# Kernel tuning notes

Measured on AMD Instinct MI355X. Metric: run time of the kernel, lower is better.

Reference implementation:

```python
import jax, jax.numpy as jnp
import numpy as np

N_CLUSTER = 1
SIZE, RATIO = 32, 0.1


def _lin_mat(n_in, n_out):
    # bilinear, align_corners=True interpolation matrix [n_out, n_in]
    src = np.arange(n_out) * (n_in - 1) / (n_out - 1)
    lo = np.floor(src).astype(np.int64)
    hi = np.minimum(lo + 1, n_in - 1)
    w = (src - lo).astype(np.float32)
    M = np.zeros((n_out, n_in), np.float32)
    M[np.arange(n_out), lo] += 1.0 - w
    M[np.arange(n_out), hi] += w
    return jnp.asarray(M)


def setup_inputs() -> dict:
    key = jax.random.key(0)
    ks = jax.random.split(key, 5)
    B, D, H, W, C = 16, 128, 128, 128, 6
    inp = {
        "assp": jax.random.normal(ks[0], (B, D, H, W), jnp.float32),
        "cls_w": jax.random.normal(ks[1], (C, D), jnp.float32) * 0.05,
        "cls_b": jnp.zeros((C,), jnp.float32),
        "key_w": jax.random.normal(ks[2], (128, D), jnp.float32) * 0.05,
        "key_b": jnp.zeros((128,), jnp.float32),
        "query_w": jax.random.normal(ks[3], (C, 128, D), jnp.float32) * 0.05,
        "query_b": jnp.zeros((C, 128), jnp.float32),
    }
    rng = np.random.default_rng(0)
    idx = rng.permutation(SIZE * SIZE)[: int(SIZE * SIZE * RATIO)]  # 102 unique pixels
    inp["px"] = jnp.asarray(idx // SIZE, jnp.int32)
    inp["py"] = jnp.asarray(idx % SIZE, jnp.int32)
    return inp


def reference(assp, cls_w, cls_b, key_w, key_b, query_w, query_b, px, py):
    B, D, H, W = assp.shape
    C = cls_w.shape[0]
    # pseudo labels (torch.no_grad)
    feats = jax.lax.stop_gradient(assp)
    pseudo = jnp.einsum('bdhw,cd->bchw', feats, cls_w) + cls_b[None, :, None, None]
    mask = jnp.argmax(pseudo, axis=1)                      # [B,H,W]
    onehot = jax.nn.one_hot(mask, C, dtype=assp.dtype)      # [B,H,W,C]
    counts = onehot.sum((1, 2))                             # [B,C]
    sums = jnp.einsum('bdhw,bhwc->bcd', assp, onehot)       # masked class sums
    protoC = sums / (counts[..., None] + 1e-5)              # [B,C,D]
    protoC = jnp.where(counts[..., None] > 0, protoC, 0.0)  # zero_prototype fallback
    protos12 = jnp.broadcast_to(protoC[:, :, None, :], (B, C, 2, D)).reshape(B, 2 * C, D)

    # DomainTrain: gather sampled pixels, L2 dist to 12 prototypes, argmin, scatter replace
    feat_px = assp[:, :, px, py]                            # [B,D,Np]
    diff = protos12[:, :, None, :] - feat_px.transpose(0, 2, 1)[:, None, :, :]  # [B,12,Np,D]
    dist = jnp.linalg.norm(diff, axis=-1)                   # [B,12,Np]
    closest = jnp.argmin(dist, axis=1)                      # [B,Np]
    repl = jnp.take_along_axis(protos12, closest[..., None], axis=1)  # [B,Np,D]
    assp = assp.at[:, :, px, py].set(repl.transpose(0, 2, 1))
    protos4 = protos12.reshape(B, C, 2, D)

    # key / query attention
    keymap = jnp.einsum('bdhw,kd->bkhw', assp, key_w) + key_b[None, :, None, None]
    q = jnp.einsum('bijd,ikd->bijk', protos4, query_w) + query_b[None, :, None, :]  # [B,C,2,128]
    sim = jnp.einsum('bijk,bkhw->bijhw', q, keymap).reshape(B, 2 * C, H, W)
    simw = jax.nn.softmax(sim / (2 * C) * N_CLUSTER, axis=1).mean(axis=1)  # [B,H,W]

    weighted = assp * simw[:, None]
    x = jnp.einsum('bdhw,cd->bchw', weighted, cls_w) + cls_b[None, :, None, None]
    My = _lin_mat(H, 4 * H)
    Mx = _lin_mat(W, 4 * W)
    xup = jnp.einsum('Hh,bchw,Ww->bcHW', My, x, Mx)
    return xup
```

## Files before the change

### kernel.cpp

```cpp
#include <hip/hip_runtime.h>

namespace {

constexpr int B  = 16;
constexpr int D  = 128;
constexpr int C  = 6;
constexpr int H  = 128;
constexpr int W  = 128;
constexpr int HWC = H * W;
constexpr int HO = 512, WO = 512;

__global__ void k_mask_x(const float* __restrict__ assp,
                         const float* __restrict__ cls_w,
                         const float* __restrict__ cls_b,
                         unsigned char* __restrict__ mask,
                         float* __restrict__ x) {
  __shared__ float ws[C * D];
  __shared__ float bs[C];
  int tid = threadIdx.x;
  for (int i = tid; i < C * D; i += 256) ws[i] = cls_w[i];
  if (tid < C) bs[tid] = cls_b[tid];
  __syncthreads();

  int p2 = (blockIdx.x * 256 + tid) * 2;
  int b  = p2 >> 14;
  int hw = p2 & (HWC - 1);
  const float* base = assp + ((size_t)b * D) * HWC + hw;

  float acc[C][2];
#pragma unroll
  for (int c = 0; c < C; ++c) { acc[c][0] = 0.f; acc[c][1] = 0.f; }

#pragma unroll 8
  for (int d = 0; d < D; ++d) {
    const float2 v = *(const float2*)(base + (size_t)d * HWC);
#pragma unroll
    for (int c = 0; c < C; ++c) {
      float w = ws[c * D + d];
      acc[c][0] += v.x * w;
      acc[c][1] += v.y * w;
    }
  }

  unsigned char mv[2];
#pragma unroll
  for (int j = 0; j < 2; ++j) {
    float bv = acc[0][j] + bs[0]; int best = 0;
#pragma unroll
    for (int c = 1; c < C; ++c) {
      float v = acc[c][j] + bs[c];
      if (v > bv) { bv = v; best = c; }
    }
    mv[j] = (unsigned char)best;
  }
  uchar2 m2; m2.x = mv[0]; m2.y = mv[1];
  *(uchar2*)(mask + p2) = m2;

  const float inv12 = 1.0f / 12.0f;
  float* xb = x + ((size_t)b * C) * HWC + hw;
#pragma unroll
  for (int c = 0; c < C; ++c) {
    float2 o;
    o.x = acc[c][0] * inv12 + bs[c];
    o.y = acc[c][1] * inv12 + bs[c];
    *(float2*)(xb + (size_t)c * HWC) = o;
  }
}

__global__ void k_proto(const float* __restrict__ assp,
                        const unsigned char* __restrict__ mask,
                        float* __restrict__ protoC) {
  int d = blockIdx.x;
  int b = blockIdx.y;
  int tid = threadIdx.x;
  const float* base = assp + ((size_t)b * D + d) * HWC;
  const unsigned char* mb = mask + (size_t)b * HWC;

  float s[C]  = {0.f, 0.f, 0.f, 0.f, 0.f, 0.f};
  int   cn[C] = {0, 0, 0, 0, 0, 0};
  for (int hw = tid * 4; hw < HWC; hw += 256 * 4) {
    float4 v = *(const float4*)(base + hw);
    uchar4 m = *(const uchar4*)(mb + hw);
#pragma unroll
    for (int c = 0; c < C; ++c) {
      bool e0 = (m.x == c), e1 = (m.y == c), e2 = (m.z == c), e3 = (m.w == c);
      s[c] += (e0 ? v.x : 0.f) + (e1 ? v.y : 0.f)
            + (e2 ? v.z : 0.f) + (e3 ? v.w : 0.f);
      cn[c] += (int)e0 + (int)e1 + (int)e2 + (int)e3;
    }
  }

  float cf[C];
#pragma unroll
  for (int c = 0; c < C; ++c) cf[c] = (float)cn[c];
#pragma unroll
  for (int off = 32; off >= 1; off >>= 1) {
#pragma unroll
    for (int c = 0; c < C; ++c) {
      s[c]  += __shfl_xor(s[c],  off, 64);
      cf[c] += __shfl_xor(cf[c], off, 64);
    }
  }
  __shared__ float red_s[C][4];
  __shared__ float red_c[C][4];
  int lane = tid & 63, wv = tid >> 6;
  if (lane == 0) {
#pragma unroll
    for (int c = 0; c < C; ++c) { red_s[c][wv] = s[c]; red_c[c][wv] = cf[c]; }
  }
  __syncthreads();
  if (tid < C) {
    float sum = red_s[tid][0] + red_s[tid][1] + red_s[tid][2] + red_s[tid][3];
    float cnt = red_c[tid][0] + red_c[tid][1] + red_c[tid][2] + red_c[tid][3];
    float pv = (cnt > 0.f) ? sum / (cnt + 1e-5f) : 0.f;
    protoC[((size_t)b * C + tid) * D + d] = pv;
  }
}

__global__ void k_replace_patch(const float* __restrict__ assp,
                                const float* __restrict__ protoC,
                                const float* __restrict__ cls_w,
                                const float* __restrict__ cls_b,
                                const int* __restrict__ px,
                                const int* __restrict__ py,
                                int P,
                                float* __restrict__ x) {
  int bp = blockIdx.x;
  int b = bp / P, p = bp % P;
  int hw = px[p] * W + py[p];
  int lane = threadIdx.x;
  const float* fbase = assp + ((size_t)b * D) * HWC + hw;
  const float* pr = protoC + (size_t)b * C * D;

  float f0 = fbase[(size_t)lane * HWC];
  float f1 = fbase[(size_t)(lane + 64) * HWC];

  float ds[C];
#pragma unroll
  for (int c = 0; c < C; ++c) {
    float d0 = pr[c * D + lane]      - f0;
    float d1 = pr[c * D + lane + 64] - f1;
    float t = d0 * d0 + d1 * d1;
#pragma unroll
    for (int off = 32; off >= 1; off >>= 1) t += __shfl_xor(t, off, 64);
    ds[c] = t;
  }
  int best = 0; float bv = ds[0];
#pragma unroll
  for (int c = 1; c < C; ++c)
    if (ds[c] < bv) { bv = ds[c]; best = c; }

  float v0 = pr[best * D + lane];
  float v1 = pr[best * D + lane + 64];

  float myx = 0.f;
#pragma unroll
  for (int c = 0; c < C; ++c) {
    float t = v0 * cls_w[c * D + lane] + v1 * cls_w[c * D + lane + 64];
#pragma unroll
    for (int off = 32; off >= 1; off >>= 1) t += __shfl_xor(t, off, 64);
    float val = t * (1.0f / 12.0f) + cls_b[c];
    if (lane == c) myx = val;
  }
  if (lane < C) x[((size_t)b * C + lane) * HWC + hw] = myx;
}

__global__ void k_up(const float* __restrict__ x, float* __restrict__ out) {
  int t = blockIdx.x * 256 + threadIdx.x;
  int i = t * 4;
  int X  = i & (WO - 1);
  int Y  = (i >> 9) & (HO - 1);
  int bc = i >> 18;

  double sy = (double)(Y * (H - 1)) / (double)(HO - 1);
  int y0 = (int)sy;
  float wy = (float)(sy - (double)y0);
  int y1 = y0 + 1; if (y1 > H - 1) y1 = H - 1;

  const float* r0 = x + (size_t)bc * HWC + y0 * W;
  const float* r1 = x + (size_t)bc * HWC + y1 * W;

  float o[4];
#pragma unroll
  for (int j = 0; j < 4; ++j) {
    int Xj = X + j;
    double sx = (double)(Xj * (W - 1)) / (double)(WO - 1);
    int x0 = (int)sx;
    float wx = (float)(sx - (double)x0);
    int x1 = x0 + 1; if (x1 > W - 1) x1 = W - 1;

    float v00 = r0[x0], v01 = r0[x1], v10 = r1[x0], v11 = r1[x1];
    o[j] = (1.f - wy) * ((1.f - wx) * v00 + wx * v01)
         +        wy  * ((1.f - wx) * v10 + wx * v11);
  }
  float4 o4; o4.x = o[0]; o4.y = o[1]; o4.z = o[2]; o4.w = o[3];
  *(float4*)(out + i) = o4;
}

}

extern "C" void kernel_launch(void* const* d_in, const int* in_sizes, int n_in,
                              void* d_out, int out_size, void* d_ws, size_t ws_size,
                              hipStream_t stream) {
  const float* assp  = (const float*)d_in[0];
  const float* cls_w = (const float*)d_in[1];
  const float* cls_b = (const float*)d_in[2];
  const int*   px    = (const int*)d_in[7];
  const int*   py    = (const int*)d_in[8];
  const int    P     = in_sizes[7];

  char* ws = (char*)d_ws;
  unsigned char* mask   = (unsigned char*)ws;
  float*         protoC = (float*)(ws + 262144);
  float*         x      = (float*)(ws + 262144 + 49152);

  float* out = (float*)d_out;

  k_mask_x<<<B * HWC / 512, 256, 0, stream>>>(assp, cls_w, cls_b, mask, x);
  k_proto<<<dim3(D, B), 256, 0, stream>>>(assp, mask, protoC);
  k_replace_patch<<<B * P, 64, 0, stream>>>(assp, protoC, cls_w, cls_b, px, py, P, x);
  k_up<<<(B * C * HO * WO) / 1024, 256, 0, stream>>>(x, out);
}
```

Measured before the change: 293.9 us.

## Fuse mask/logit and prototype accumulation into one tiled pass over assp

Merges the classifier/argmax kernel and the per-class prototype reduction into a single kernel that stages 64-pixel by 128-channel tiles of assp in shared memory. Each tile is used both for the logits and for the masked class sums, so the second full read of assp is removed. Partial sums and counts go to global memory through atomics after a memset, and the prototype division moves into the patch kernel. The cost is extra shared-memory traffic, several block barriers per tile, and atomic contention that makes the float sums order-dependent.

```diff
diff --git a/kernel.cpp b/kernel.cpp
--- a/kernel.cpp
+++ b/kernel.cpp
@@ -9,157 +9,172 @@
 constexpr int W  = 128;
 constexpr int HWC = H * W;
 constexpr int HO = 512, WO = 512;
-
-__global__ void k_mask_x(const float* __restrict__ assp,
-                         const float* __restrict__ cls_w,
-                         const float* __restrict__ cls_b,
-                         unsigned char* __restrict__ mask,
-                         float* __restrict__ x) {
+constexpr int TILE = 64;
+constexpr int TPB  = 8;
+
+__global__ __launch_bounds__(256) void k_fused(const float* __restrict__ assp,
+                                               const float* __restrict__ cls_w,
+                                               const float* __restrict__ cls_b,
+                                               float* __restrict__ sums,
+                                               int* __restrict__ counts,
+                                               float* __restrict__ x) {
+  __shared__ float tile[D * TILE];
+  __shared__ float red[4 * C * TILE];
   __shared__ float ws[C * D];
   __shared__ float bs[C];
-  int tid = threadIdx.x;
-  for (int i = tid; i < C * D; i += 256) ws[i] = cls_w[i];
-  if (tid < C) bs[tid] = cls_b[tid];
+
+  const int t  = threadIdx.x;
+  const int b  = blockIdx.y;
+  for (int i = t; i < C * D; i += 256) ws[i] = cls_w[i];
+  if (t < C) bs[t] = cls_b[t];
+
+  const int lane = t & 63;
+  const int wv   = t >> 6;
+  const int d2b  = t & 127;
+  const int h2b  = t >> 7;
+  const int d1   = t >> 5;
+  const int px2  = (t & 31) * 2;
+
+  float acc2b[C] = {0.f, 0.f, 0.f, 0.f, 0.f, 0.f};
+  int   cnt_run  = 0;
+
   __syncthreads();
 
-  int p2 = (blockIdx.x * 256 + tid) * 2;
-  int b  = p2 >> 14;
-  int hw = p2 & (HWC - 1);
-  const float* base = assp + ((size_t)b * D) * HWC + hw;
-
-  float acc[C][2];
-#pragma unroll
-  for (int c = 0; c < C; ++c) { acc[c][0] = 0.f; acc[c][1] = 0.f; }
-
-#pragma unroll 8
-  for (int d = 0; d < D; ++d) {
-    const float2 v = *(const float2*)(base + (size_t)d * HWC);
+  for (int it = 0; it < TPB; ++it) {
+    const int hw0 = (blockIdx.x * TPB + it) * TILE;
+    const float* base = assp + ((size_t)b * D) * HWC + hw0;
+
+    float2 v[16];
+#pragma unroll
+    for (int j = 0; j < 16; ++j) {
+      int d = d1 + 8 * j;
+      v[j] = *(const float2*)(base + (size_t)d * HWC + px2);
+    }
+#pragma unroll
+    for (int j = 0; j < 16; ++j) {
+      int d = d1 + 8 * j;
+      *(float2*)&tile[d * TILE + (px2 ^ (d & 62))] = v[j];
+    }
+    __syncthreads();
+
+    {
+      float a[C] = {0.f, 0.f, 0.f, 0.f, 0.f, 0.f};
+#pragma unroll
+      for (int dd = 0; dd < 32; ++dd) {
+        int d = wv * 32 + dd;
+        float vv = tile[d * TILE + (lane ^ (d & 62))];
+#pragma unroll
+        for (int c = 0; c < C; ++c) a[c] += vv * ws[c * D + d];
+      }
+#pragma unroll
+      for (int c = 0; c < C; ++c) red[(wv * C + c) * TILE + lane] = a[c];
+    }
+    __syncthreads();
+
+    int cls;
+    {
+      float s[C];
+#pragma unroll
+      for (int c = 0; c < C; ++c)
+        s[c] = red[(0 * C + c) * TILE + lane] + red[(1 * C + c) * TILE + lane]
+             + red[(2 * C + c) * TILE + lane] + red[(3 * C + c) * TILE + lane];
+      float bv = s[0] + bs[0]; cls = 0;
+#pragma unroll
+      for (int c = 1; c < C; ++c) {
+        float pv = s[c] + bs[c];
+        if (pv > bv) { bv = pv; cls = c; }
+      }
+      if (wv == 0) {
+        const float inv12 = 1.0f / 12.0f;
+        float* xb = x + ((size_t)b * C) * HWC + hw0 + lane;
+#pragma unroll
+        for (int c = 0; c < C; ++c) xb[(size_t)c * HWC] = s[c] * inv12 + bs[c];
+#pragma unroll
+        for (int c = 0; c < C; ++c) {
+          unsigned long long m = __ballot(cls == c);
+          if (lane == c) cnt_run += (int)__popcll(m);
+        }
+      }
+    }
+
+#pragma unroll
+    for (int i = 0; i < 32; ++i) {
+      int px = h2b * 32 + i;
+      float vv = tile[d2b * TILE + (px ^ (d2b & 62))];
+      int c = __shfl(cls, px, 64);
+#pragma unroll
+      for (int cc = 0; cc < C; ++cc) acc2b[cc] += (c == cc) ? vv : 0.f;
+    }
+    __syncthreads();
+  }
+
+  float* part = red;
+  if (h2b == 1) {
+#pragma unroll
+    for (int c = 0; c < C; ++c) part[c * D + d2b] = acc2b[c];
+  }
+  __syncthreads();
+  if (h2b == 0) {
 #pragma unroll
     for (int c = 0; c < C; ++c) {
-      float w = ws[c * D + d];
-      acc[c][0] += v.x * w;
-      acc[c][1] += v.y * w;
-    }
-  }
-
-  unsigned char mv[2];
-#pragma unroll
-  for (int j = 0; j < 2; ++j) {
-    float bv = acc[0][j] + bs[0]; int best = 0;
-#pragma unroll
-    for (int c = 1; c < C; ++c) {
-      float v = acc[c][j] + bs[c];
-      if (v > bv) { bv = v; best = c; }
-    }
-    mv[j] = (unsigned char)best;
-  }
-  uchar2 m2; m2.x = mv[0]; m2.y = mv[1];
-  *(uchar2*)(mask + p2) = m2;
-
-  const float inv12 = 1.0f / 12.0f;
-  float* xb = x + ((size_t)b * C) * HWC + hw;
-#pragma unroll
-  for (int c = 0; c < C; ++c) {
-    float2 o;
-    o.x = acc[c][0] * inv12 + bs[c];
-    o.y = acc[c][1] * inv12 + bs[c];
-    *(float2*)(xb + (size_t)c * HWC) = o;
-  }
-}
-
-__global__ void k_proto(const float* __restrict__ assp,
-                        const unsigned char* __restrict__ mask,
-                        float* __restrict__ protoC) {
-  int d = blockIdx.x;
-  int b = blockIdx.y;
-  int tid = threadIdx.x;
-  const float* base = assp + ((size_t)b * D + d) * HWC;
-  const unsigned char* mb = mask + (size_t)b * HWC;
-
-  float s[C]  = {0.f, 0.f, 0.f, 0.f, 0.f, 0.f};
-  int   cn[C] = {0, 0, 0, 0, 0, 0};
-  for (int hw = tid * 4; hw < HWC; hw += 256 * 4) {
-    float4 v = *(const float4*)(base + hw);
-    uchar4 m = *(const uchar4*)(mb + hw);
-#pragma unroll
-    for (int c = 0; c < C; ++c) {
-      bool e0 = (m.x == c), e1 = (m.y == c), e2 = (m.z == c), e3 = (m.w == c);
-      s[c] += (e0 ? v.x : 0.f) + (e1 ? v.y : 0.f)
-            + (e2 ? v.z : 0.f) + (e3 ? v.w : 0.f);
-      cn[c] += (int)e0 + (int)e1 + (int)e2 + (int)e3;
-    }
-  }
-
-  float cf[C];
-#pragma unroll
-  for (int c = 0; c < C; ++c) cf[c] = (float)cn[c];
-#pragma unroll
-  for (int off = 32; off >= 1; off >>= 1) {
-#pragma unroll
-    for (int c = 0; c < C; ++c) {
-      s[c]  += __shfl_xor(s[c],  off, 64);
-      cf[c] += __shfl_xor(cf[c], off, 64);
-    }
-  }
-  __shared__ float red_s[C][4];
-  __shared__ float red_c[C][4];
-  int lane = tid & 63, wv = tid >> 6;
-  if (lane == 0) {
-#pragma unroll
-    for (int c = 0; c < C; ++c) { red_s[c][wv] = s[c]; red_c[c][wv] = cf[c]; }
-  }
-  __syncthreads();
-  if (tid < C) {
-    float sum = red_s[tid][0] + red_s[tid][1] + red_s[tid][2] + red_s[tid][3];
-    float cnt = red_c[tid][0] + red_c[tid][1] + red_c[tid][2] + red_c[tid][3];
-    float pv = (cnt > 0.f) ? sum / (cnt + 1e-5f) : 0.f;
-    protoC[((size_t)b * C + tid) * D + d] = pv;
-  }
-}
-
-__global__ void k_replace_patch(const float* __restrict__ assp,
-                                const float* __restrict__ protoC,
-                                const float* __restrict__ cls_w,
-                                const float* __restrict__ cls_b,
-                                const int* __restrict__ px,
-                                const int* __restrict__ py,
-                                int P,
-                                float* __restrict__ x) {
+      float s = acc2b[c] + part[c * D + d2b];
+      atomicAdd(&sums[((size_t)b * C + c) * D + d2b], s);
+    }
+  }
+  if (wv == 0 && lane < C) atomicAdd(&counts[b * C + lane], cnt_run);
+}
+
+__global__ void k_patch(const float* __restrict__ assp,
+                        const float* __restrict__ sums,
+                        const int* __restrict__ counts,
+                        const float* __restrict__ cls_w,
+                        const float* __restrict__ cls_b,
+                        const int* __restrict__ px,
+                        const int* __restrict__ py,
+                        int P,
+                        float* __restrict__ x) {
   int bp = blockIdx.x;
   int b = bp / P, p = bp % P;
   int hw = px[p] * W + py[p];
   int lane = threadIdx.x;
   const float* fbase = assp + ((size_t)b * D) * HWC + hw;
-  const float* pr = protoC + (size_t)b * C * D;
 
   float f0 = fbase[(size_t)lane * HWC];
   float f1 = fbase[(size_t)(lane + 64) * HWC];
 
-  float ds[C];
+  float pv0[C], pv1[C], ds[C];
 #pragma unroll
   for (int c = 0; c < C; ++c) {
-    float d0 = pr[c * D + lane]      - f0;
-    float d1 = pr[c * D + lane + 64] - f1;
-    float t = d0 * d0 + d1 * d1;
-#pragma unroll
-    for (int off = 32; off >= 1; off >>= 1) t += __shfl_xor(t, off, 64);
-    ds[c] = t;
+    float cnt = (float)counts[b * C + c];
+    float s0 = sums[((size_t)b * C + c) * D + lane];
+    float s1 = sums[((size_t)b * C + c) * D + lane + 64];
+    float q0 = (cnt > 0.f) ? s0 / (cnt + 1e-5f) : 0.f;
+    float q1 = (cnt > 0.f) ? s1 / (cnt + 1e-5f) : 0.f;
+    pv0[c] = q0; pv1[c] = q1;
+    float e0 = q0 - f0, e1 = q1 - f1;
+    float tt = e0 * e0 + e1 * e1;
+#pragma unroll
+    for (int off = 32; off >= 1; off >>= 1) tt += __shfl_xor(tt, off, 64);
+    ds[c] = tt;
   }
   int best = 0; float bv = ds[0];
 #pragma unroll
   for (int c = 1; c < C; ++c)
     if (ds[c] < bv) { bv = ds[c]; best = c; }
 
-  float v0 = pr[best * D + lane];
-  float v1 = pr[best * D + lane + 64];
+  float v0 = 0.f, v1 = 0.f;
+#pragma unroll
+  for (int c = 0; c < C; ++c) {
+    if (best == c) { v0 = pv0[c]; v1 = pv1[c]; }
+  }
 
   float myx = 0.f;
 #pragma unroll
   for (int c = 0; c < C; ++c) {
-    float t = v0 * cls_w[c * D + lane] + v1 * cls_w[c * D + lane + 64];
-#pragma unroll
-    for (int off = 32; off >= 1; off >>= 1) t += __shfl_xor(t, off, 64);
-    float val = t * (1.0f / 12.0f) + cls_b[c];
+    float tt = v0 * cls_w[c * D + lane] + v1 * cls_w[c * D + lane + 64];
+#pragma unroll
+    for (int off = 32; off >= 1; off >>= 1) tt += __shfl_xor(tt, off, 64);
+    float val = tt * (1.0f / 12.0f) + cls_b[c];
     if (lane == c) myx = val;
   }
   if (lane < C) x[((size_t)b * C + lane) * HWC + hw] = myx;
@@ -210,14 +225,15 @@
   const int    P     = in_sizes[7];
 
   char* ws = (char*)d_ws;
-  unsigned char* mask   = (unsigned char*)ws;
-  float*         protoC = (float*)(ws + 262144);
-  float*         x      = (float*)(ws + 262144 + 49152);
+  float* sums   = (float*)ws;
+  int*   counts = (int*)(ws + 49152);
+  float* x      = (float*)(ws + 65536);
 
   float* out = (float*)d_out;
 
-  k_mask_x<<<B * HWC / 512, 256, 0, stream>>>(assp, cls_w, cls_b, mask, x);
-  k_proto<<<dim3(D, B), 256, 0, stream>>>(assp, mask, protoC);
-  k_replace_patch<<<B * P, 64, 0, stream>>>(assp, protoC, cls_w, cls_b, px, py, P, x);
+  hipMemsetAsync(ws, 0, 49152 + 384, stream);
+  k_fused<<<dim3(HWC / (TILE * TPB), B), 256, 0, stream>>>(assp, cls_w, cls_b,
+                                                           sums, counts, x);
+  k_patch<<<B * P, 64, 0, stream>>>(assp, sums, counts, cls_w, cls_b, px, py, P, x);
   k_up<<<(B * C * HO * WO) / 1024, 256, 0, stream>>>(x, out);
 }
```

Measured after the change: 277.1 us. -5.7%, faster.
